# Kernel optimization log

Hardware: AMD Instinct MI355X
Metric: run time of the kernel (lower is better)

The kernel has to match this reference:

```python
import jax, jax.numpy as jnp
import numpy as np

N = 8192        # number of nodes
IN_CH = 256     # in_channels
OUT_CH = 256    # out_channels


def setup_inputs() -> dict:
    key = jax.random.key(0)
    k1, k2, k3, k4 = jax.random.split(key, 4)
    A = jax.random.normal(k1, (N, N), dtype=jnp.float32)
    # degree-like matrix: only its diagonal matters; keep it strictly positive
    D = jax.random.uniform(k2, (N, N), dtype=jnp.float32, minval=0.5, maxval=2.0)
    H = jax.random.normal(k3, (N, IN_CH), dtype=jnp.float32)
    W = jax.random.normal(k4, (IN_CH, OUT_CH), dtype=jnp.float32)  # nn.Parameter, normal_() init
    return {"A": A, "D": D, "H": H, "W": W}


def reference(A, D, H, W):
    # Original: D_ = diag(diag(rsqrt(D))); T = D_ @ A @ D_ @ H @ W
    # diag-matrix matmuls are mathematically row/column scalings; same math, no O(n^3) diag mm.
    d = jax.lax.rsqrt(jnp.diagonal(D))          # [N], rsqrt of diagonal entries
    A_norm = A * d[:, None] * d[None, :]        # D^-1/2 A D^-1/2, fused elementwise
    return (A_norm @ H) @ W                     # [N, OUT_CH]
```

## Files before the change

kernel.cpp:

```cpp
#include <hip/hip_runtime.h>
#include <hip/hip_bf16.h>

#define NN 8192
#define CH 256

typedef float f32x4 __attribute__((ext_vector_type(4)));
typedef __bf16 bf16x8 __attribute__((ext_vector_type(8)));

union FragU { uint4 u; bf16x8 h; };

static __device__ __forceinline__ unsigned short f2bf(float f) {
  union { float f; unsigned int u; } v; v.f = f;
  unsigned int x = v.u;
  return (unsigned short)((x + 0x7fffu + ((x >> 16) & 1u)) >> 16);
}

#if defined(__has_builtin)
#if __has_builtin(__builtin_amdgcn_global_load_lds)
#define HAVE_GLL 1
#endif
#endif

#ifdef HAVE_GLL
static __device__ __forceinline__ void gload16(const void* g, void* l) {
  __builtin_amdgcn_global_load_lds(
      (const __attribute__((address_space(1))) void*)(unsigned long long)(g),
      (__attribute__((address_space(3))) void*)(unsigned int)(unsigned long long)(l),
      16, 0, 0);
}
#endif

static __device__ __forceinline__ unsigned int cvtpk(float a, float b) {
  unsigned int r;
  asm("v_cvt_pk_bf16_f32 %0, %1, %2" : "=v"(r) : "v"(a), "v"(b));
  return r;
}

#define WAITV(n) asm volatile("s_waitcnt vmcnt(" #n ")" ::: "memory")
#define BARRIER() __builtin_amdgcn_s_barrier()

__global__ __launch_bounds__(256) void k_prep(const float* __restrict__ Hm,
                                              const float* __restrict__ Dm,
                                              const float* __restrict__ Wm,
                                              unsigned short* __restrict__ HT,
                                              unsigned short* __restrict__ WT) {
  __shared__ float tile[64][65];
  int bx = blockIdx.x, t = threadIdx.x;
  bool isH = bx < 512;
  int b = isH ? bx : bx - 512;
  int r0 = (b >> 2) * 64;
  int j0 = (b & 3) * 64;
  const float* src = isH ? Hm : Wm;

  int r = t >> 2;
  int cq = (t & 3) * 16;
  float dval = isH ? rsqrtf(Dm[(size_t)(r0 + r) * (NN + 1)]) : 1.0f;
  const float* p = src + (size_t)(r0 + r) * CH + j0 + cq;
#pragma unroll
  for (int u = 0; u < 4; ++u) {
    float4 v = *(const float4*)(p + u * 4);
    tile[r][cq + u * 4 + 0] = v.x * dval;
    tile[r][cq + u * 4 + 1] = v.y * dval;
    tile[r][cq + u * 4 + 2] = v.z * dval;
    tile[r][cq + u * 4 + 3] = v.w * dval;
  }
  __syncthreads();
  int j = t >> 2;
  int kq = (t & 3) * 16;
  __align__(16) unsigned short ov[16];
#pragma unroll
  for (int i = 0; i < 16; ++i) ov[i] = f2bf(tile[kq + i][j]);
  unsigned short* dst = isH ? (HT + (size_t)(j0 + j) * NN + r0 + kq)
                            : (WT + (size_t)(j0 + j) * CH + r0 + kq);
  *(uint4*)dst = *(uint4*)ov;
  *(uint4*)(dst + 8) = *(uint4*)(ov + 8);
}

template <int SK>
__global__ __launch_bounds__(512, 1) void k_gemm1(const float* __restrict__ A,
                                                  const unsigned short* __restrict__ HT,
                                                  float* __restrict__ P) {
  constexpr int KC = NN / SK;
  constexpr int NIT = KC / 64;
  __shared__ float Asf[2][8192];
  const int bx = blockIdx.x;
  const int strip = bx / SK, s = bx % SK;
  const int i0 = strip * 128;
  const size_t kbase = (size_t)s * KC;
  const int t = threadIdx.x, l = t & 63, w = t >> 6;
  const int lan = l & 15, quad = l >> 4;
  const int wr = w >> 2, wc = w & 3;

  const char* Ag = (const char*)A
      + ((size_t)(i0 + (t >> 4)) * NN + kbase) * 4
      + (size_t)((((t & 15) * 16) ^ (((t >> 4) & 7) * 16)));

  const unsigned short* Bb = HT + (size_t)(wc * 64 + lan) * NN + kbase + quad * 8;

  FragU b0[8], b1[8];
  f32x4 acc[4][4];
#pragma unroll
  for (int mt = 0; mt < 4; ++mt)
#pragma unroll
    for (int nt = 0; nt < 4; ++nt)
#pragma unroll
      for (int c = 0; c < 4; ++c) acc[mt][nt][c] = 0.0f;

  auto stage = [&](int kt, int buf) {
    const char* g = Ag + (size_t)kt * 256;
#ifdef HAVE_GLL
#pragma unroll
    for (int u = 0; u < 4; ++u)
      gload16(g + (size_t)u * ((size_t)32 * NN * 4), &Asf[buf][u * 2048 + w * 256]);
#else
    float4 tv[4];
#pragma unroll
    for (int u = 0; u < 4; ++u)
      tv[u] = *(const float4*)(g + (size_t)u * ((size_t)32 * NN * 4));
#pragma unroll
    for (int u = 0; u < 4; ++u)
      *(float4*)((char*)&Asf[buf][0] + (size_t)(u * 512 + t) * 16) = tv[u];
    asm volatile("s_waitcnt lgkmcnt(0)" ::: "memory");
#endif
  };

  auto loadB = [&](FragU (&dst)[8], int kt) {
    const unsigned short* p = Bb + (size_t)kt * 64;
#pragma unroll
    for (int ss = 0; ss < 2; ++ss)
#pragma unroll
      for (int nt = 0; nt < 4; ++nt)
        dst[ss * 4 + nt].u = *(const uint4*)(p + (size_t)nt * 16 * NN + ss * 32);
  };

  const int sw = (lan & 7) * 16;
  auto compute = [&](FragU (&b)[8], const char* Ab) {
#pragma unroll
    for (int ss = 0; ss < 2; ++ss) {
      FragU af[4];
#pragma unroll
      for (int mt = 0; mt < 4; ++mt) {
        const int row = wr * 64 + mt * 16 + lan;
        const char* rp = Ab + row * 256;
        const int x = ss * 128 + quad * 32;
        float4 va = *(const float4*)(rp + ((x) ^ sw));
        float4 vb = *(const float4*)(rp + ((x + 16) ^ sw));
        af[mt].u.x = cvtpk(va.x, va.y);
        af[mt].u.y = cvtpk(va.z, va.w);
        af[mt].u.z = cvtpk(vb.x, vb.y);
        af[mt].u.w = cvtpk(vb.z, vb.w);
      }
#pragma unroll
      for (int mt = 0; mt < 4; ++mt)
#pragma unroll
        for (int nt = 0; nt < 4; ++nt)
          acc[mt][nt] = __builtin_amdgcn_mfma_f32_16x16x32_bf16(af[mt].h, b[ss * 4 + nt].h,
                                                                acc[mt][nt], 0, 0, 0);
    }
  };

  stage(0, 0);
  loadB(b0, 0);
#pragma unroll 1
  for (int kt = 0; kt < NIT; kt += 2) {
    stage(kt + 1, 1);
    loadB(b1, kt + 1);
    WAITV(12);
    BARRIER();
    compute(b0, (const char*)&Asf[0][0]);
    BARRIER();
    if (kt + 2 < NIT) {
      stage(kt + 2, 0);
      loadB(b0, kt + 2);
      WAITV(12);
    } else {
      WAITV(0);
    }
    BARRIER();
    compute(b1, (const char*)&Asf[1][0]);
    BARRIER();
  }

  float* Pp = P + ((size_t)s * NN + i0) * CH;
#pragma unroll
  for (int mt = 0; mt < 4; ++mt)
#pragma unroll
    for (int nt = 0; nt < 4; ++nt)
#pragma unroll
      for (int r = 0; r < 4; ++r)
        Pp[(size_t)(wr * 64 + mt * 16 + quad * 4 + r) * CH + wc * 64 + nt * 16 + lan]
            = acc[mt][nt][r];
}

template <int SK>
__global__ __launch_bounds__(256) void k_gemm2(const float* __restrict__ P,
                                               const float* __restrict__ Dm,
                                               const unsigned short* __restrict__ WT,
                                               float* __restrict__ out) {
  __shared__ unsigned short Gs[16][264];
  const int bx = blockIdx.x, t = threadIdx.x, l = t & 63, w = t >> 6;
  const int lan = l & 15, quad = l >> 4;
  const int i0 = bx * 16;
  {
    const int r = t >> 4, c0 = (t & 15) * 16;
    float dval = rsqrtf(Dm[(size_t)(i0 + r) * (NN + 1)]);
    const float* pp = P + (size_t)(i0 + r) * CH + c0;
    __align__(16) unsigned short g[16];
#pragma unroll
    for (int u = 0; u < 4; ++u) {
      float sx = 0.f, sy = 0.f, sz = 0.f, sw2 = 0.f;
#pragma unroll
      for (int s = 0; s < SK; ++s) {
        float4 v = *(const float4*)(pp + (size_t)s * NN * CH + u * 4);
        sx += v.x; sy += v.y; sz += v.z; sw2 += v.w;
      }
      g[u * 4 + 0] = f2bf(sx * dval);
      g[u * 4 + 1] = f2bf(sy * dval);
      g[u * 4 + 2] = f2bf(sz * dval);
      g[u * 4 + 3] = f2bf(sw2 * dval);
    }
    *(uint4*)&Gs[r][c0] = *(uint4*)g;
    *(uint4*)&Gs[r][c0 + 8] = *(uint4*)(g + 8);
  }
  __syncthreads();
  const int j0 = w * 64;
  f32x4 acc[4];
#pragma unroll
  for (int nt = 0; nt < 4; ++nt)
#pragma unroll
    for (int c = 0; c < 4; ++c) acc[nt][c] = 0.0f;
#pragma unroll
  for (int ks = 0; ks < 8; ++ks) {
    FragU af;
    af.u = *(const uint4*)&Gs[lan][ks * 32 + quad * 8];
#pragma unroll
    for (int nt = 0; nt < 4; ++nt) {
      FragU bw;
      bw.u = *(const uint4*)&WT[(size_t)(j0 + nt * 16 + lan) * CH + ks * 32 + quad * 8];
      acc[nt] = __builtin_amdgcn_mfma_f32_16x16x32_bf16(af.h, bw.h, acc[nt], 0, 0, 0);
    }
  }
#pragma unroll
  for (int nt = 0; nt < 4; ++nt)
#pragma unroll
    for (int r = 0; r < 4; ++r)
      out[(size_t)(i0 + quad * 4 + r) * CH + j0 + nt * 16 + lan] = acc[nt][r];
}

extern "C" void kernel_launch(void* const* d_in, const int* in_sizes, int n_in,
                              void* d_out, int out_size, void* d_ws, size_t ws_size,
                              hipStream_t stream) {
  const float* A  = (const float*)d_in[0];
  const float* Dm = (const float*)d_in[1];
  const float* Hm = (const float*)d_in[2];
  const float* Wm = (const float*)d_in[3];
  float* out = (float*)d_out;
  char* ws = (char*)d_ws;
  unsigned short* HT = (unsigned short*)ws;
  unsigned short* WT = (unsigned short*)(ws + (size_t)4194304);
  float* P = (float*)(ws + (size_t)4194304 + 131072);

  const size_t base = 4194304 + 131072;
  const size_t needS4 = base + (size_t)4 * NN * CH * 4;

  hipLaunchKernelGGL(k_prep, dim3(528), dim3(256), 0, stream, Hm, Dm, Wm, HT, WT);
  if (ws_size >= needS4) {
    hipLaunchKernelGGL((k_gemm1<4>), dim3(256), dim3(512), 0, stream, A, HT, P);
    hipLaunchKernelGGL((k_gemm2<4>), dim3(512), dim3(256), 0, stream, P, Dm, WT, out);
  } else {
    hipLaunchKernelGGL((k_gemm1<2>), dim3(128), dim3(512), 0, stream, A, HT, P);
    hipLaunchKernelGGL((k_gemm2<2>), dim3(512), dim3(256), 0, stream, P, Dm, WT, out);
  }
}
```

Measured before the change: 522.7 us.

## Fuse both GEMMs into one kernel with 32-row strips and no split-K

Replaces the split-K first GEMM plus the separate reduce-and-second-GEMM kernel with a single kernel. Each block owns 32 rows across the full K dimension, scales the result by rsqrt(D) into shared memory, then multiplies by W in place. This removes the partial-sum workspace writes and reads and one launch. In exchange, each block does far less work per A tile (a 32x256 output instead of 128x256), so every block reads the full H^T column set and reuse of H is lower. Each block also has fewer loads in flight per iteration.

```diff
diff --git a/kernel.cpp b/kernel.cpp
--- a/kernel.cpp
+++ b/kernel.cpp
@@ -76,72 +76,61 @@
   *(uint4*)(dst + 8) = *(uint4*)(ov + 8);
 }
 
-template <int SK>
-__global__ __launch_bounds__(512, 1) void k_gemm1(const float* __restrict__ A,
+__global__ __launch_bounds__(512, 1) void k_fused(const float* __restrict__ A,
+                                                  const float* __restrict__ Dm,
                                                   const unsigned short* __restrict__ HT,
-                                                  float* __restrict__ P) {
-  constexpr int KC = NN / SK;
-  constexpr int NIT = KC / 64;
-  __shared__ float Asf[2][8192];
-  const int bx = blockIdx.x;
-  const int strip = bx / SK, s = bx % SK;
-  const int i0 = strip * 128;
-  const size_t kbase = (size_t)s * KC;
-  const int t = threadIdx.x, l = t & 63, w = t >> 6;
+                                                  const unsigned short* __restrict__ WT,
+                                                  float* __restrict__ out) {
+  constexpr int NIT = NN / 64;
+  __shared__ float Asf[2][2048];
+  __shared__ unsigned short Gs[32][264];
+  __shared__ float dsh[32];
+  const int bx = blockIdx.x, t = threadIdx.x, l = t & 63, w = t >> 6;
   const int lan = l & 15, quad = l >> 4;
-  const int wr = w >> 2, wc = w & 3;
-
-  const char* Ag = (const char*)A
-      + ((size_t)(i0 + (t >> 4)) * NN + kbase) * 4
-      + (size_t)((((t & 15) * 16) ^ (((t >> 4) & 7) * 16)));
-
-  const unsigned short* Bb = HT + (size_t)(wc * 64 + lan) * NN + kbase + quad * 8;
-
-  FragU b0[8], b1[8];
-  f32x4 acc[4][4];
-#pragma unroll
-  for (int mt = 0; mt < 4; ++mt)
-#pragma unroll
-    for (int nt = 0; nt < 4; ++nt)
+  const int i0 = bx * 32;
+
+  const char* Ag = (const char*)A + (size_t)(i0 + (t >> 4)) * NN * 4
+                   + (size_t)(((t & 15) ^ ((t >> 4) & 7)) * 16);
+  const unsigned short* Bb = HT + (size_t)(w * 32 + lan) * NN + quad * 8;
+
+  if (t < 32) dsh[t] = rsqrtf(Dm[(size_t)(i0 + t) * (NN + 1)]);
+
+  FragU b0[4], b1[4];
+  f32x4 acc[2][2];
+#pragma unroll
+  for (int mt = 0; mt < 2; ++mt)
+#pragma unroll
+    for (int nt = 0; nt < 2; ++nt)
 #pragma unroll
       for (int c = 0; c < 4; ++c) acc[mt][nt][c] = 0.0f;
 
   auto stage = [&](int kt, int buf) {
-    const char* g = Ag + (size_t)kt * 256;
 #ifdef HAVE_GLL
-#pragma unroll
-    for (int u = 0; u < 4; ++u)
-      gload16(g + (size_t)u * ((size_t)32 * NN * 4), &Asf[buf][u * 2048 + w * 256]);
+    gload16(Ag + (size_t)kt * 256, (char*)&Asf[buf][0] + t * 16);
 #else
-    float4 tv[4];
-#pragma unroll
-    for (int u = 0; u < 4; ++u)
-      tv[u] = *(const float4*)(g + (size_t)u * ((size_t)32 * NN * 4));
-#pragma unroll
-    for (int u = 0; u < 4; ++u)
-      *(float4*)((char*)&Asf[buf][0] + (size_t)(u * 512 + t) * 16) = tv[u];
+    float4 tv = *(const float4*)(Ag + (size_t)kt * 256);
+    *(float4*)((char*)&Asf[buf][0] + t * 16) = tv;
     asm volatile("s_waitcnt lgkmcnt(0)" ::: "memory");
 #endif
   };
 
-  auto loadB = [&](FragU (&dst)[8], int kt) {
+  auto loadB = [&](FragU (&dst)[4], int kt) {
     const unsigned short* p = Bb + (size_t)kt * 64;
 #pragma unroll
     for (int ss = 0; ss < 2; ++ss)
 #pragma unroll
-      for (int nt = 0; nt < 4; ++nt)
-        dst[ss * 4 + nt].u = *(const uint4*)(p + (size_t)nt * 16 * NN + ss * 32);
+      for (int nt = 0; nt < 2; ++nt)
+        dst[ss * 2 + nt].u = *(const uint4*)(p + (size_t)nt * 16 * NN + ss * 32);
   };
 
   const int sw = (lan & 7) * 16;
-  auto compute = [&](FragU (&b)[8], const char* Ab) {
+  auto compute = [&](FragU (&b)[4], const char* Ab) {
 #pragma unroll
     for (int ss = 0; ss < 2; ++ss) {
-      FragU af[4];
-#pragma unroll
-      for (int mt = 0; mt < 4; ++mt) {
-        const int row = wr * 64 + mt * 16 + lan;
-        const char* rp = Ab + row * 256;
+      FragU af[2];
+#pragma unroll
+      for (int mt = 0; mt < 2; ++mt) {
+        const char* rp = Ab + (mt * 16 + lan) * 256;
         const int x = ss * 128 + quad * 32;
         float4 va = *(const float4*)(rp + ((x) ^ sw));
         float4 vb = *(const float4*)(rp + ((x + 16) ^ sw));
@@ -151,10 +140,10 @@
         af[mt].u.w = cvtpk(vb.z, vb.w);
       }
 #pragma unroll
-      for (int mt = 0; mt < 4; ++mt)
-#pragma unroll
-        for (int nt = 0; nt < 4; ++nt)
-          acc[mt][nt] = __builtin_amdgcn_mfma_f32_16x16x32_bf16(af[mt].h, b[ss * 4 + nt].h,
+      for (int mt = 0; mt < 2; ++mt)
+#pragma unroll
+        for (int nt = 0; nt < 2; ++nt)
+          acc[mt][nt] = __builtin_amdgcn_mfma_f32_16x16x32_bf16(af[mt].h, b[ss * 2 + nt].h,
                                                                 acc[mt][nt], 0, 0, 0);
     }
   };
@@ -165,14 +154,14 @@
   for (int kt = 0; kt < NIT; kt += 2) {
     stage(kt + 1, 1);
     loadB(b1, kt + 1);
-    WAITV(12);
+    WAITV(5);
     BARRIER();
     compute(b0, (const char*)&Asf[0][0]);
     BARRIER();
     if (kt + 2 < NIT) {
       stage(kt + 2, 0);
       loadB(b0, kt + 2);
-      WAITV(12);
+      WAITV(5);
     } else {
       WAITV(0);
     }
@@ -181,70 +170,39 @@
     BARRIER();
   }
 
-  float* Pp = P + ((size_t)s * NN + i0) * CH;
-#pragma unroll
-  for (int mt = 0; mt < 4; ++mt)
-#pragma unroll
-    for (int nt = 0; nt < 4; ++nt)
-#pragma unroll
-      for (int r = 0; r < 4; ++r)
-        Pp[(size_t)(wr * 64 + mt * 16 + quad * 4 + r) * CH + wc * 64 + nt * 16 + lan]
-            = acc[mt][nt][r];
-}
-
-template <int SK>
-__global__ __launch_bounds__(256) void k_gemm2(const float* __restrict__ P,
-                                               const float* __restrict__ Dm,
-                                               const unsigned short* __restrict__ WT,
-                                               float* __restrict__ out) {
-  __shared__ unsigned short Gs[16][264];
-  const int bx = blockIdx.x, t = threadIdx.x, l = t & 63, w = t >> 6;
-  const int lan = l & 15, quad = l >> 4;
-  const int i0 = bx * 16;
-  {
-    const int r = t >> 4, c0 = (t & 15) * 16;
-    float dval = rsqrtf(Dm[(size_t)(i0 + r) * (NN + 1)]);
-    const float* pp = P + (size_t)(i0 + r) * CH + c0;
-    __align__(16) unsigned short g[16];
-#pragma unroll
-    for (int u = 0; u < 4; ++u) {
-      float sx = 0.f, sy = 0.f, sz = 0.f, sw2 = 0.f;
-#pragma unroll
-      for (int s = 0; s < SK; ++s) {
-        float4 v = *(const float4*)(pp + (size_t)s * NN * CH + u * 4);
-        sx += v.x; sy += v.y; sz += v.z; sw2 += v.w;
+#pragma unroll
+  for (int mt = 0; mt < 2; ++mt)
+#pragma unroll
+    for (int nt = 0; nt < 2; ++nt)
+#pragma unroll
+      for (int r = 0; r < 4; ++r) {
+        const int row = mt * 16 + quad * 4 + r;
+        Gs[row][w * 32 + nt * 16 + lan] = f2bf(acc[mt][nt][r] * dsh[row]);
       }
-      g[u * 4 + 0] = f2bf(sx * dval);
-      g[u * 4 + 1] = f2bf(sy * dval);
-      g[u * 4 + 2] = f2bf(sz * dval);
-      g[u * 4 + 3] = f2bf(sw2 * dval);
-    }
-    *(uint4*)&Gs[r][c0] = *(uint4*)g;
-    *(uint4*)&Gs[r][c0 + 8] = *(uint4*)(g + 8);
-  }
   __syncthreads();
-  const int j0 = w * 64;
-  f32x4 acc[4];
+
+  const int r0w = (w & 1) * 16, j0c = (w >> 1) * 64;
+  f32x4 o[4];
 #pragma unroll
   for (int nt = 0; nt < 4; ++nt)
 #pragma unroll
-    for (int c = 0; c < 4; ++c) acc[nt][c] = 0.0f;
+    for (int c = 0; c < 4; ++c) o[nt][c] = 0.0f;
 #pragma unroll
   for (int ks = 0; ks < 8; ++ks) {
     FragU af;
-    af.u = *(const uint4*)&Gs[lan][ks * 32 + quad * 8];
+    af.u = *(const uint4*)&Gs[r0w + lan][ks * 32 + quad * 8];
 #pragma unroll
     for (int nt = 0; nt < 4; ++nt) {
       FragU bw;
-      bw.u = *(const uint4*)&WT[(size_t)(j0 + nt * 16 + lan) * CH + ks * 32 + quad * 8];
-      acc[nt] = __builtin_amdgcn_mfma_f32_16x16x32_bf16(af.h, bw.h, acc[nt], 0, 0, 0);
+      bw.u = *(const uint4*)&WT[(size_t)(j0c + nt * 16 + lan) * CH + ks * 32 + quad * 8];
+      o[nt] = __builtin_amdgcn_mfma_f32_16x16x32_bf16(af.h, bw.h, o[nt], 0, 0, 0);
     }
   }
 #pragma unroll
   for (int nt = 0; nt < 4; ++nt)
 #pragma unroll
     for (int r = 0; r < 4; ++r)
-      out[(size_t)(i0 + quad * 4 + r) * CH + j0 + nt * 16 + lan] = acc[nt][r];
+      out[(size_t)(i0 + r0w + quad * 4 + r) * CH + j0c + nt * 16 + lan] = o[nt][r];
 }
 
 extern "C" void kernel_launch(void* const* d_in, const int* in_sizes, int n_in,
@@ -258,17 +216,7 @@
   char* ws = (char*)d_ws;
   unsigned short* HT = (unsigned short*)ws;
   unsigned short* WT = (unsigned short*)(ws + (size_t)4194304);
-  float* P = (float*)(ws + (size_t)4194304 + 131072);
-
-  const size_t base = 4194304 + 131072;
-  const size_t needS4 = base + (size_t)4 * NN * CH * 4;
 
   hipLaunchKernelGGL(k_prep, dim3(528), dim3(256), 0, stream, Hm, Dm, Wm, HT, WT);
-  if (ws_size >= needS4) {
-    hipLaunchKernelGGL((k_gemm1<4>), dim3(256), dim3(512), 0, stream, A, HT, P);
-    hipLaunchKernelGGL((k_gemm2<4>), dim3(512), dim3(256), 0, stream, P, Dm, WT, out);
-  } else {
-    hipLaunchKernelGGL((k_gemm1<2>), dim3(128), dim3(512), 0, stream, A, HT, P);
-    hipLaunchKernelGGL((k_gemm2<2>), dim3(512), dim3(256), 0, stream, P, Dm, WT, out);
-  }
-}
+  hipLaunchKernelGGL(k_fused, dim3(256), dim3(512), 0, stream, A, Dm, HT, WT, out);
+}
```

Measured after the change: 580.2 us. 1.11x slower.
